# Optimization experiments

Hardware: AMD Instinct MI355X
Metric: run time of the kernel (lower is better)

Reference implementation:

```python
import jax, jax.numpy as jnp
import numpy as np
from jax import lax

NUM_HEADS = 4
KEY_DEPTHS = 32
ATTN_CH = 32
OUT_CH = 64
IN_CH = 32
KSIZE = 3


def circ_conv3d(x, w, b=None):
    # x: (B,C,D,H,W), w: (O,I,k,k,k); circular padding keeps spatial dims.
    k = w.shape[-1]
    p = k // 2
    if p > 0:
        x = jnp.pad(x, ((0, 0), (0, 0), (p, p), (p, p), (p, p)), mode='wrap')
    y = lax.conv_general_dilated(x, w, (1, 1, 1), 'VALID',
                                 dimension_numbers=('NCDHW', 'OIDHW', 'NCDHW'))
    if b is not None:
        y = y + b[None, :, None, None, None]
    return y


def setup_inputs() -> dict:
    key = jax.random.key(0)
    k1, k2, k3, k4, k5 = jax.random.split(key, 5)
    x = jax.random.normal(k1, (2, IN_CH, 16, 16, 16), dtype=jnp.float32)
    fan = IN_CH * KSIZE ** 3
    w_init = jax.random.normal(k2, (OUT_CH - ATTN_CH, IN_CH, KSIZE, KSIZE, KSIZE), dtype=jnp.float32) / np.sqrt(fan)
    w_qkv = jax.random.normal(k3, (2 * KEY_DEPTHS + ATTN_CH, IN_CH, KSIZE, KSIZE, KSIZE), dtype=jnp.float32) / np.sqrt(fan)
    w_out = jax.random.normal(k4, (ATTN_CH, ATTN_CH, 1, 1, 1), dtype=jnp.float32) / np.sqrt(ATTN_CH)
    b_out = jax.random.normal(k5, (ATTN_CH,), dtype=jnp.float32) * 0.01
    return {'x': x, 'w_init': w_init, 'w_qkv': w_qkv, 'w_out': w_out, 'b_out': b_out}


def reference(x, w_init, w_qkv, w_out, b_out):
    out = circ_conv3d(x, w_init)                      # (b, out-attn, w,h,d)
    b, _, w, h, d = out.shape
    qkv = circ_conv3d(x, w_qkv)                       # (b, 2dk+dv, w,h,d)
    q, k, v = jnp.split(qkv, [KEY_DEPTHS, 2 * KEY_DEPTHS], axis=1)
    dk_h = KEY_DEPTHS // NUM_HEADS
    dv_h = ATTN_CH // NUM_HEADS
    N = w * h * d
    scale = dk_h ** -0.5
    fq = q.reshape(b, NUM_HEADS, dk_h, N) * scale     # (b,H,dk_h,N)
    fk = k.reshape(b, NUM_HEADS, dk_h, N)
    fv = v.reshape(b, NUM_HEADS, dv_h, N)
    logits = jnp.einsum('bhcn,bhcm->bhnm', fq, fk)    # (b,H,N,N)
    weights = jax.nn.softmax(logits, axis=-1)
    attn = jnp.einsum('bhnm,bhvm->bhnv', weights, fv)  # (b,H,N,dv_h)
    # Faithful to torch: a pure reshape (memory reinterpretation), not a transpose.
    attn = attn.reshape(b, NUM_HEADS, dv_h, w, h, d)
    attn = attn.reshape(b, NUM_HEADS * dv_h, w, h, d)  # combine heads
    attn = circ_conv3d(attn, w_out, b_out)             # 1x1x1 conv
    return jnp.concatenate([out, attn], axis=1)
```

## Files before the change

### kernel.cpp

```cpp
#include <hip/hip_runtime.h>


typedef short short8 __attribute__((ext_vector_type(8)));
typedef float float4v __attribute__((ext_vector_type(4)));
typedef unsigned short ushort_t;
typedef unsigned int uint_t;

__device__ inline ushort_t f2bf(float x) {
  uint_t u = __builtin_bit_cast(uint_t, x);
  u += 0x7FFFu + ((u >> 16) & 1u);
  return (ushort_t)(u >> 16);
}

__device__ inline uint_t cvtpk(float lo, float hi) {
  uint_t r;
  asm("v_cvt_pk_bf16_f32 %0, %1, %2" : "=v"(r) : "v"(lo), "v"(hi));
  return r;
}

__global__ __launch_bounds__(256, 1) void kConv(const float* __restrict__ x,
                                                const float* __restrict__ w_init,
                                                const float* __restrict__ w_qkv,
                                                float* __restrict__ out,
                                                ushort_t* __restrict__ Qbf,
                                                ushort_t* __restrict__ Kbf,
                                                ushort_t* __restrict__ VtTp) {
  __shared__ ushort_t wl[27 * 512];
  __shared__ ushort_t xs[256 * 32];
  __shared__ float xsf[128 * 34];
  int tid = threadIdx.x;
  int w = tid >> 6, lane = tid & 63;
  int quad = lane >> 4, nl = lane & 15;
  int bx = blockIdx.x;
  int oq = bx & 7;
  int z = (bx >> 3) & 15;
  int b = bx >> 7;

  const float* wsrc = (oq < 2) ? (w_init + (size_t)oq * 16 * 864)
                               : (w_qkv + (size_t)(oq - 2) * 16 * 864);
  const float QS = 0.35355339059327373f * 1.4426950408889634f;
  float wscale = (oq == 2 || oq == 3) ? QS : 1.0f;
#pragma unroll
  for (int i = 0; i < 14; ++i) {
    int idx4 = i * 256 + tid;
    if (idx4 < 3456) {
      float4 v = *(const float4*)(wsrc + (size_t)idx4 * 4);
      float vv[4] = {v.x, v.y, v.z, v.w};
#pragma unroll
      for (int k = 0; k < 4; ++k) {
        int e = idx4 * 4 + k;
        int tap = e % 27;
        int rest = e / 27;
        int ic = rest & 31;
        int oo = rest >> 5;
        wl[tap * 512 + ((ic >> 3) * 16 + oo) * 8 + (ic & 7)] = f2bf(vv[k] * wscale);
      }
    }
  }

  float4v acc[4];
#pragma unroll
  for (int st = 0; st < 4; ++st) acc[st] = (float4v){0.f, 0.f, 0.f, 0.f};
  int y0 = w * 4;

  for (int kz = 0; kz < 3; ++kz) {
    int zr = (z + kz + 15) & 15;
#pragma unroll
    for (int h = 0; h < 2; ++h) {
      __syncthreads();
      int rloc = tid & 127;
      int ich = tid >> 7;
#pragma unroll
      for (int icq = 0; icq < 16; ++icq) {
        int ic = ich * 16 + icq;
        xsf[rloc * 34 + ic] = x[((size_t)(b * 32 + ic) * 16 + zr) * 256 + h * 128 + rloc];
      }
      __syncthreads();
#pragma unroll
      for (int r = 0; r < 2; ++r) {
        int slot = r * 256 + tid;
        int sl = slot >> 2;
        int icg = slot & 3;
        ushort_t tmp[8];
#pragma unroll
        for (int jj = 0; jj < 8; ++jj) tmp[jj] = f2bf(xsf[sl * 34 + icg * 8 + jj]);
        *(short8*)(xs + (h * 128 + sl) * 32 + icg * 8) = *(short8*)tmp;
      }
    }
    __syncthreads();

#pragma unroll
    for (int kyx = 0; kyx < 9; ++kyx) {
      int ky = kyx / 3, kx = kyx % 3;
      int tap = kz * 9 + kyx;
      short8 afrag = *(const short8*)(wl + tap * 512 + lane * 8);
      int xsh = (nl + kx + 15) & 15;
#pragma unroll
      for (int st = 0; st < 4; ++st) {
        int yy = (y0 + st + ky + 15) & 15;
        short8 bfrag = *(const short8*)(xs + (yy * 16 + xsh) * 32 + quad * 8);
        acc[st] = __builtin_amdgcn_mfma_f32_16x16x32_bf16(afrag, bfrag, acc[st], 0, 0, 0);
      }
    }
  }

#pragma unroll
  for (int st = 0; st < 4; ++st) {
    int y = y0 + st;
    int s = z * 256 + y * 16 + nl;
    int mperm = 2 * nl + (y & 1);
#pragma unroll
    for (int r = 0; r < 4; ++r) {
      float val = acc[st][r];
      int oo = (oq & 1) * 16 + quad * 4 + r;
      if (oq < 2) {
        out[(size_t)(b * 64 + oo) * 4096 + s] = val;
      } else if (oq < 4) {
        int h = oo >> 3, c = oo & 7;
        Qbf[((size_t)(b * 4 + h) * 4096 + s) * 8 + c] = f2bf(val);
      } else if (oq < 6) {
        int h = oo >> 3, c = oo & 7;
        Kbf[((size_t)(b * 4 + h) * 4096 + s) * 8 + c] = f2bf(val);
      } else {
        int h = oo >> 3, c = oo & 7;
        VtTp[((size_t)(b * 4 + h) * 8 + c) * 4096 + (size_t)(s & ~31) + mperm] = f2bf(val);
      }
    }
  }
}

template <int KSP>
__global__ __launch_bounds__(256) void kAttn(const ushort_t* __restrict__ Qbf,
                                             const ushort_t* __restrict__ Kbf,
                                             const ushort_t* __restrict__ VtTp,
                                             float* __restrict__ pacc,
                                             float* __restrict__ pl) {
  const int NCH = 128 / KSP;
  __shared__ ushort_t Plds[4 * 2 * 2 * 640];
  int tid = threadIdx.x;
  int w = tid >> 6, lane = tid & 63;
  int id = blockIdx.x * 4 + w;
  int bh = id / (KSP * 128);
  int rem = id % (KSP * 128);
  int ksp = rem >> 7;
  int ntile = rem & 127;
  int n0 = ntile * 32;
  int quad = lane >> 4, nl = lane & 15;
  int l31 = lane & 31;
  int v = nl;

  short8 z8 = {};
  short8 q0f = *(const short8*)(Qbf + ((size_t)bh * 4096 + n0 + nl) * 8);
  short8 q1f = *(const short8*)(Qbf + ((size_t)bh * 4096 + n0 + 16 + nl) * 8);
  short8 aq0A = (quad == 0) ? q0f : z8;
  short8 aq0B = (quad == 1) ? q0f : z8;
  short8 aq1A = (quad == 0) ? q1f : z8;
  short8 aq1B = (quad == 1) ? q1f : z8;

  short8 ones8;
#pragma unroll
  for (int i = 0; i < 8; ++i) ones8[i] = (short)0x3F80;

  const ushort_t* Krows = Kbf + ((size_t)bh * 4096 + ksp * (4096 / KSP)) * 8;
  const ushort_t* Vrow = VtTp + ((size_t)bh * 8 + (v < 8 ? v : 0)) * 4096
                         + ksp * (4096 / KSP) + quad * 8;
  ushort_t* P0 = Plds + (w * 2 + 0) * 2 * 640;
  ushort_t* P1 = Plds + (w * 2 + 1) * 2 * 640;

  float4v acc0 = {}, acc1 = {};

#define QKEXP(mi, bkr)                                                         \
  {                                                                            \
    float4v s00 = __builtin_amdgcn_mfma_f32_16x16x32_bf16(                     \
        aq0A, bkr, (float4v){0.f, 0.f, 0.f, 0.f}, 0, 0, 0);                    \
    float4v s01 = __builtin_amdgcn_mfma_f32_16x16x32_bf16(                     \
        aq0B, bkr, (float4v){0.f, 0.f, 0.f, 0.f}, 0, 0, 0);                    \
    float4v s10 = __builtin_amdgcn_mfma_f32_16x16x32_bf16(                     \
        aq1A, bkr, (float4v){0.f, 0.f, 0.f, 0.f}, 0, 0, 0);                    \
    float4v s11 = __builtin_amdgcn_mfma_f32_16x16x32_bf16(                     \
        aq1B, bkr, (float4v){0.f, 0.f, 0.f, 0.f}, 0, 0, 0);                    \
    uint_t* Pt0 = (uint_t*)(P0 + ((mi) & 1) * 640);                            \
    uint_t* Pt1 = (uint_t*)(P1 + ((mi) & 1) * 640);                            \
    _Pragma("unroll") for (int r = 0; r < 4; ++r) {                            \
      Pt0[(quad * 4 + r) * 20 + nl] =                                          \
          cvtpk(__builtin_amdgcn_exp2f(s00[r]), __builtin_amdgcn_exp2f(s01[r]));\
      Pt1[(quad * 4 + r) * 20 + nl] =                                          \
          cvtpk(__builtin_amdgcn_exp2f(s10[r]), __builtin_amdgcn_exp2f(s11[r]));\
    }                                                                          \
  }

#define PVSTEP(a2, bv, accv)                                                   \
  {                                                                            \
    short8 b2 = (v < 8) ? (bv) : ((v == 8) ? ones8 : z8);                      \
    accv = __builtin_amdgcn_mfma_f32_16x16x32_bf16(a2, b2, accv, 0, 0, 0);     \
  }

  short8 bk = *(const short8*)(Krows + (size_t)l31 * 8);
  QKEXP(0, bk)
  bk = *(const short8*)(Krows + (size_t)(32 + l31) * 8);

#pragma unroll 2
  for (int mi = 1; mi < NCH; ++mi) {
    int pb = ((mi - 1) & 1) * 640;
    short8 a20 = *(const short8*)(P0 + pb + nl * 40 + quad * 8);
    short8 a21 = *(const short8*)(P1 + pb + nl * 40 + quad * 8);
    short8 bv = *(const short8*)(Vrow + (mi - 1) * 32);
    QKEXP(mi, bk)
    int nxt = ((mi + 1) & (NCH - 1)) * 32;
    bk = *(const short8*)(Krows + (size_t)(nxt + l31) * 8);
    PVSTEP(a20, bv, acc0)
    PVSTEP(a21, bv, acc1)
  }
  {
    int pb = ((NCH - 1) & 1) * 640;
    short8 a20 = *(const short8*)(P0 + pb + nl * 40 + quad * 8);
    short8 a21 = *(const short8*)(P1 + pb + nl * 40 + quad * 8);
    short8 bv = *(const short8*)(Vrow + (NCH - 1) * 32);
    PVSTEP(a20, bv, acc0)
    PVSTEP(a21, bv, acc1)
  }
#undef QKEXP
#undef PVSTEP

#pragma unroll
  for (int r = 0; r < 4; ++r) {
    int rq = quad * 4 + r;
    int rowg0 = bh * 4096 + n0 + rq;
    int rowg1 = rowg0 + 16;
    if (v < 8) {
      pacc[((size_t)rowg0 * KSP + ksp) * 8 + v] = acc0[r];
      pacc[((size_t)rowg1 * KSP + ksp) * 8 + v] = acc1[r];
    } else if (v == 8) {
      pl[(size_t)rowg0 * KSP + ksp] = acc0[r];
      pl[(size_t)rowg1 * KSP + ksp] = acc1[r];
    }
  }
}

template <int KSP>
__global__ __launch_bounds__(256) void kOut(const float* __restrict__ pacc,
                                            const float* __restrict__ pl,
                                            const float* __restrict__ w_out,
                                            const float* __restrict__ b_out,
                                            float* __restrict__ out) {
  __shared__ float M[32 * 64];
  int bx = blockIdx.x;
  int b = bx >> 6;
  int sp0 = (bx & 63) * 64;
  int t = threadIdx.x;

  {
    int ci = t >> 3, nsub = t & 7;
    int h = ci >> 3, tt = ci & 7;
    int n = tt * 512 + (sp0 >> 3) + nsub;
    size_t row = (size_t)(b * 4 + h) * 4096 + n;
    float l = 0.f;
#pragma unroll
    for (int s = 0; s < KSP; ++s) l += pl[row * KSP + s];
    float rl = 1.0f / l;
    float m[8];
#pragma unroll
    for (int c = 0; c < 8; ++c) m[c] = 0.f;
#pragma unroll
    for (int s = 0; s < KSP; ++s) {
      const float4 p0 = *(const float4*)(pacc + (row * KSP + s) * 8);
      const float4 p1 = *(const float4*)(pacc + (row * KSP + s) * 8 + 4);
      m[0] += p0.x; m[1] += p0.y; m[2] += p0.z; m[3] += p0.w;
      m[4] += p1.x; m[5] += p1.y; m[6] += p1.z; m[7] += p1.w;
    }
    float4 o0 = {m[0] * rl, m[1] * rl, m[2] * rl, m[3] * rl};
    float4 o1 = {m[4] * rl, m[5] * rl, m[6] * rl, m[7] * rl};
    *(float4*)(M + ci * 64 + nsub * 8) = o0;
    *(float4*)(M + ci * 64 + nsub * 8 + 4) = o1;
  }
  __syncthreads();

  {
    int spl = t & 63;
    int cog = t >> 6;
    float a[32];
#pragma unroll
    for (int ci = 0; ci < 32; ++ci) a[ci] = M[ci * 64 + spl];
#pragma unroll
    for (int oo = 0; oo < 8; ++oo) {
      int co = cog * 8 + oo;
      float r = b_out[co];
#pragma unroll
      for (int ci = 0; ci < 32; ++ci) r = fmaf(w_out[co * 32 + ci], a[ci], r);
      out[(size_t)(b * 64 + 32 + co) * 4096 + sp0 + spl] = r;
    }
  }
}

extern "C" void kernel_launch(void* const* d_in, const int* in_sizes, int n_in,
                              void* d_out, int out_size, void* d_ws, size_t ws_size,
                              hipStream_t stream) {
  const float* x      = (const float*)d_in[0];
  const float* w_init = (const float*)d_in[1];
  const float* w_qkv  = (const float*)d_in[2];
  const float* w_out  = (const float*)d_in[3];
  const float* b_out  = (const float*)d_in[4];
  float* out = (float*)d_out;

  const size_t fixed = 3 * 524288;
  int KSP = (ws_size >= fixed + (size_t)8 * (1048576 + 131072)) ? 8 : 4;

  ushort_t* Qbf = (ushort_t*)d_ws;
  ushort_t* Kbf = Qbf + 262144;
  ushort_t* VtTp = Kbf + 262144;
  float* pacc = (float*)(VtTp + 262144);
  float* pl = pacc + (size_t)KSP * 262144;

  kConv <<<256, 256, 0, stream>>>(x, w_init, w_qkv, out, Qbf, Kbf, VtTp);
  if (KSP == 8) {
    kAttn<8><<<2048, 256, 0, stream>>>(Qbf, Kbf, VtTp, pacc, pl);
    kOut<8> <<<128, 256, 0, stream>>>(pacc, pl, w_out, b_out, out);
  } else {
    kAttn<4><<<1024, 256, 0, stream>>>(Qbf, Kbf, VtTp, pacc, pl);
    kOut<4> <<<128, 256, 0, stream>>>(pacc, pl, w_out, b_out, out);
  }
}
```

Baseline: 102.5 us.

## Pad V^T to 16 rows with a ones row, and vectorize the x staging loads

The V^T buffer is widened from 8 to 16 rows per head, and the conv kernel fills row 8 with bf16 ones and rows 9-15 with zeros. The attention kernel can then load its PV B-operand directly with no per-lane select between V, ones and zero. This removes two vector selects per PV step in the hot loop, at the cost of double the V workspace and extra global writes in kConv. The x input staging in kConv also switches from scalar loads to float4 loads.

```diff
diff --git a/kernel.cpp b/kernel.cpp
--- a/kernel.cpp
+++ b/kernel.cpp
@@ -58,6 +58,21 @@
     }
   }
 
+  if (oq == 7) {
+#pragma unroll
+    for (int i = 0; i < 4; ++i) {
+      int idx = i * 256 + tid;
+      int row = idx >> 5;
+      int h = row >> 3, rr = row & 7;
+      ushort_t val = (rr == 0) ? (ushort_t)0x3F80 : (ushort_t)0;
+      short8 v8;
+#pragma unroll
+      for (int j = 0; j < 8; ++j) v8[j] = (short)val;
+      *(short8*)(VtTp + ((size_t)((b * 4 + h) * 16) + 8 + rr) * 4096
+                 + z * 256 + (idx & 31) * 8) = v8;
+    }
+  }
+
   float4v acc[4];
 #pragma unroll
   for (int st = 0; st < 4; ++st) acc[st] = (float4v){0.f, 0.f, 0.f, 0.f};
@@ -68,12 +83,16 @@
 #pragma unroll
     for (int h = 0; h < 2; ++h) {
       __syncthreads();
-      int rloc = tid & 127;
-      int ich = tid >> 7;
-#pragma unroll
-      for (int icq = 0; icq < 16; ++icq) {
-        int ic = ich * 16 + icq;
-        xsf[rloc * 34 + ic] = x[((size_t)(b * 32 + ic) * 16 + zr) * 256 + h * 128 + rloc];
+#pragma unroll
+      for (int i = 0; i < 4; ++i) {
+        int q = i * 256 + tid;
+        int ic = q >> 5;
+        int sq = q & 31;
+        float4 v = *(const float4*)(x + ((size_t)(b * 32 + ic) * 16 + zr) * 256
+                                      + h * 128 + sq * 4);
+        float vv[4] = {v.x, v.y, v.z, v.w};
+#pragma unroll
+        for (int j = 0; j < 4; ++j) xsf[(sq * 4 + j) * 34 + ic] = vv[j];
       }
       __syncthreads();
 #pragma unroll
@@ -123,7 +142,7 @@
         Kbf[((size_t)(b * 4 + h) * 4096 + s) * 8 + c] = f2bf(val);
       } else {
         int h = oo >> 3, c = oo & 7;
-        VtTp[((size_t)(b * 4 + h) * 8 + c) * 4096 + (size_t)(s & ~31) + mperm] = f2bf(val);
+        VtTp[((size_t)((b * 4 + h) * 16) + c) * 4096 + (size_t)(s & ~31) + mperm] = f2bf(val);
       }
     }
   }
@@ -157,12 +176,8 @@
   short8 aq1A = (quad == 0) ? q1f : z8;
   short8 aq1B = (quad == 1) ? q1f : z8;
 
-  short8 ones8;
-#pragma unroll
-  for (int i = 0; i < 8; ++i) ones8[i] = (short)0x3F80;
-
   const ushort_t* Krows = Kbf + ((size_t)bh * 4096 + ksp * (4096 / KSP)) * 8;
-  const ushort_t* Vrow = VtTp + ((size_t)bh * 8 + (v < 8 ? v : 0)) * 4096
+  const ushort_t* Vrow = VtTp + ((size_t)(bh * 16 + v)) * 4096
                          + ksp * (4096 / KSP) + quad * 8;
   ushort_t* P0 = Plds + (w * 2 + 0) * 2 * 640;
   ushort_t* P1 = Plds + (w * 2 + 1) * 2 * 640;
@@ -189,12 +204,6 @@
     }                                                                          \
   }
 
-#define PVSTEP(a2, bv, accv)                                                   \
-  {                                                                            \
-    short8 b2 = (v < 8) ? (bv) : ((v == 8) ? ones8 : z8);                      \
-    accv = __builtin_amdgcn_mfma_f32_16x16x32_bf16(a2, b2, accv, 0, 0, 0);     \
-  }
-
   short8 bk = *(const short8*)(Krows + (size_t)l31 * 8);
   QKEXP(0, bk)
   bk = *(const short8*)(Krows + (size_t)(32 + l31) * 8);
@@ -208,19 +217,18 @@
     QKEXP(mi, bk)
     int nxt = ((mi + 1) & (NCH - 1)) * 32;
     bk = *(const short8*)(Krows + (size_t)(nxt + l31) * 8);
-    PVSTEP(a20, bv, acc0)
-    PVSTEP(a21, bv, acc1)
+    acc0 = __builtin_amdgcn_mfma_f32_16x16x32_bf16(a20, bv, acc0, 0, 0, 0);
+    acc1 = __builtin_amdgcn_mfma_f32_16x16x32_bf16(a21, bv, acc1, 0, 0, 0);
   }
   {
     int pb = ((NCH - 1) & 1) * 640;
     short8 a20 = *(const short8*)(P0 + pb + nl * 40 + quad * 8);
     short8 a21 = *(const short8*)(P1 + pb + nl * 40 + quad * 8);
     short8 bv = *(const short8*)(Vrow + (NCH - 1) * 32);
-    PVSTEP(a20, bv, acc0)
-    PVSTEP(a21, bv, acc1)
+    acc0 = __builtin_amdgcn_mfma_f32_16x16x32_bf16(a20, bv, acc0, 0, 0, 0);
+    acc1 = __builtin_amdgcn_mfma_f32_16x16x32_bf16(a21, bv, acc1, 0, 0, 0);
   }
 #undef QKEXP
-#undef PVSTEP
 
 #pragma unroll
   for (int r = 0; r < 4; ++r) {
@@ -302,13 +310,13 @@
   const float* b_out  = (const float*)d_in[4];
   float* out = (float*)d_out;
 
-  const size_t fixed = 3 * 524288;
+  const size_t fixed = 2 * 524288 + 1048576;
   int KSP = (ws_size >= fixed + (size_t)8 * (1048576 + 131072)) ? 8 : 4;
 
   ushort_t* Qbf = (ushort_t*)d_ws;
   ushort_t* Kbf = Qbf + 262144;
   ushort_t* VtTp = Kbf + 262144;
-  float* pacc = (float*)(VtTp + 262144);
+  float* pacc = (float*)(VtTp + 524288);
   float* pl = pacc + (size_t)KSP * 262144;
 
   kConv <<<256, 256, 0, stream>>>(x, w_init, w_qkv, out, Qbf, Kbf, VtTp);
```

Measured after the change: 107.0 us. 1.04x slower.
